# Performance work log

Hardware: AMD Instinct MI355X
Metric: run time of the kernel (lower is better)

The kernel has to match this reference:

```python
import jax, jax.numpy as jnp
import numpy as np

B, N, D, H, K, P, E = 4, 2048, 512, 8, 9, 8, 4
HID = 2048  # mlp_ratio * dim


def _ln(x, g, b, eps):
    m = x.mean(-1, keepdims=True)
    v = ((x - m) ** 2).mean(-1, keepdims=True)
    return (x - m) / jnp.sqrt(v + eps) * g + b


def _l2(x):
    # F.normalize(dim=-1)
    return x / jnp.maximum(jnp.linalg.norm(x, axis=-1, keepdims=True), 1e-12)


def _rope(t, pos):
    # t: [B,H,L,hd], rotate-half rotary embedding
    half = t.shape[-1] // 2
    inv = 1.0 / (10000.0 ** (jnp.arange(half, dtype=jnp.float32) / half))
    ang = pos[:, None].astype(jnp.float32) * inv  # [L, half]
    c, s = jnp.cos(ang), jnp.sin(ang)
    t1, t2 = t[..., :half], t[..., half:]
    return jnp.concatenate([t1 * c - t2 * s, t1 * s + t2 * c], axis=-1)


def setup_inputs() -> dict:
    key = jax.random.key(0)
    ks = jax.random.split(key, 12)
    w = lambda k, shape: jax.random.normal(k, shape, jnp.float32) * 0.02
    z = lambda *shape: jnp.zeros(shape, jnp.float32)
    o = lambda *shape: jnp.ones(shape, jnp.float32)
    return {
        'x': jax.random.normal(ks[0], (B, N, D), jnp.float32),
        'temperature': jnp.full((H, 1, 1), float(np.log(np.expm1(1.0 / 0.24))), jnp.float32),
        'q_w': w(ks[1], (D, D)), 'q_b': z(D),
        'kv_w': w(ks[2], (D, 2 * D)), 'kv_b': z(2 * D),
        'attn_proj_w': w(ks[3], (D, D)), 'attn_proj_b': z(D),
        'norm1_g': o(D), 'norm1_b': z(D),
        'norm2_g': o(D), 'norm2_b': z(D),
        'sr_w': w(ks[4], (D, D)), 'sr_b': z(D),  # Conv1d k=1 == pointwise linear
        'normp_g': o(D), 'normp_b': z(D),
        'router_w': w(ks[5], (D, E)), 'router_b': z(E),
        'ew1': w(ks[6], (E, D, HID)), 'eb1': z(E, HID),
        'ew2': w(ks[7], (E, HID, D)), 'eb2': z(E, D),
        'sw1': w(ks[8], (D, HID)), 'sb1': z(HID),
        'sw2': w(ks[9], (HID, D)), 'sb2': z(D),
    }


def _forward(x, temperature, q_w, q_b, kv_w, kv_b, attn_proj_w, attn_proj_b,
             norm1_g, norm1_b, norm2_g, norm2_b, sr_w, sr_b, normp_g, normp_b,
             router_w, router_b, ew1, eb1, ew2, eb2, sw1, sb1, sw2, sb2):
    Bn, Nn, Dd = x.shape
    hd = Dd // H
    scale_len = jnp.float32(np.log(K - 1 + P))  # log(local_len + pool_len)

    xn = _ln(x, norm1_g, norm1_b, 1e-6)
    q = (xn @ q_w + q_b).reshape(Bn, Nn, H, hd).transpose(0, 2, 1, 3)
    qs = _l2(q) * jax.nn.softplus(temperature) * scale_len  # [B,H,N,hd]
    kv = xn @ kv_w + kv_b
    kL = kv[..., :Dd].reshape(Bn, Nn, H, hd).transpose(0, 2, 1, 3)
    vL = kv[..., Dd:].reshape(Bn, Nn, H, hd).transpose(0, 2, 1, 3)
    pos = jnp.arange(Nn)
    qs = _rope(qs, pos)
    kL = _l2(_rope(kL, pos))

    # sliding-window local attention (qk with zero rpb; OOB positions -> -inf)
    offs = jnp.arange(K) - K // 2
    idx = jnp.arange(Nn)[:, None] + offs          # [N,K]
    valid = (idx >= 0) & (idx < Nn)
    idxc = jnp.clip(idx, 0, Nn - 1)
    kwin = kL[:, :, idxc, :]                       # [B,H,N,K,hd]
    attn_local = jnp.einsum('bhnd,bhnkd->bhnk', qs, kwin)
    attn_local = jnp.where(valid[None, None], attn_local, -jnp.inf)

    # pooled global branch: conv1x1 -> GELU -> adaptive avg pool -> LN
    xp = jax.nn.gelu(xn @ sr_w + sr_b, approximate=False)
    xp = xp.reshape(Bn, P, Nn // P, Dd).mean(2)    # AdaptiveAvgPool1d(P)
    xp = _ln(xp, normp_g, normp_b, 1e-5)
    kvp = xp @ kv_w + kv_b
    kP = kvp[..., :Dd].reshape(Bn, P, H, hd).transpose(0, 2, 1, 3)
    vP = kvp[..., Dd:].reshape(Bn, P, H, hd).transpose(0, 2, 1, 3)
    kP = _rope(kP, jnp.arange(P))
    attn_pool = jnp.einsum('bhnd,bhpd->bhnp', qs, kP)

    attn = jax.nn.softmax(jnp.concatenate([attn_local, attn_pool], -1), axis=-1)
    aL, aP = attn[..., :K], attn[..., K:]
    vwin = vL[:, :, idxc, :]
    xl = jnp.einsum('bhnk,bhnkd->bhnd', aL, vwin)
    xg = jnp.einsum('bhnp,bhpd->bhnd', aP, vP)
    attn_out = (xl + xg).transpose(0, 2, 1, 3).reshape(Bn, Nn, Dd)
    x = x + (attn_out @ attn_proj_w + attn_proj_b)

    # MoE with shared expert (dense soft gating + switch-style aux loss)
    xn2 = _ln(x, norm2_g, norm2_b, 1e-6)
    gates = jax.nn.softmax(xn2 @ router_w + router_b, axis=-1)  # [B,N,E]
    h = jax.nn.gelu(jnp.einsum('bnd,edh->bneh', xn2, ew1) + eb1, approximate=False)
    eo = jnp.einsum('bneh,ehd->bned', h, ew2) + eb2
    shared = jax.nn.gelu(xn2 @ sw1 + sb1, approximate=False) @ sw2 + sb2
    moe = jnp.einsum('bne,bned->bnd', gates, eo) + shared
    x = x + moe
    fi = jnp.mean(jax.nn.one_hot(jnp.argmax(gates, -1), E, dtype=jnp.float32), axis=(0, 1))
    Pi = jnp.mean(gates, axis=(0, 1))
    aux = jnp.float32(0.01) * E * jnp.sum(fi * Pi)
    return x, aux


def reference(x, temperature, q_w, q_b, kv_w, kv_b, attn_proj_w, attn_proj_b,
              norm1_g, norm1_b, norm2_g, norm2_b, sr_w, sr_b, normp_g, normp_b,
              router_w, router_b, ew1, eb1, ew2, eb2, sw1, sb1, sw2, sb2):
    return _forward(x, temperature, q_w, q_b, kv_w, kv_b, attn_proj_w, attn_proj_b,
                    norm1_g, norm1_b, norm2_g, norm2_b, sr_w, sr_b, normp_g, normp_b,
                    router_w, router_b, ew1, eb1, ew2, eb2, sw1, sb1, sw2, sb2)
```

## Files before the change

### kernel.cpp

```cpp
#include <hip/hip_runtime.h>
#include <hip/hip_bf16.h>
#include <math.h>

#define B_ 4
#define N_ 2048
#define D_ 512
#define H_ 8
#define HD_ 64
#define KW_ 9
#define P_ 8
#define E_ 4
#define HID_ 2048
#define TOK_ (B_*N_)

typedef __bf16 bf16x8 __attribute__((ext_vector_type(8)));
typedef float  f32x4  __attribute__((ext_vector_type(4)));

static __device__ __forceinline__ float wave_sum(float v){
#pragma unroll
  for(int off=32; off>0; off>>=1) v += __shfl_xor(v, off);
  return v;
}

static __device__ __forceinline__ float gelu_exact(float v){
  return 0.5f * v * (1.f + erff(v * 0.70710678118654752440f));
}

static __device__ __forceinline__ void split2(float v, unsigned short& h, unsigned short& l){
  __bf16 bh = (__bf16)v;
  float r = v - (float)bh;
  __bf16 bl = (__bf16)r;
  h = __builtin_bit_cast(unsigned short, bh);
  l = __builtin_bit_cast(unsigned short, bl);
}
static __device__ __forceinline__ float bf2f(unsigned short u){
  return (float)__builtin_bit_cast(__bf16, u);
}
static __device__ __forceinline__ unsigned short f2bf(float v){
  return __builtin_bit_cast(unsigned short, (__bf16)v);
}

static __device__ __forceinline__ void gload16(const unsigned short* g, unsigned short* l){
  __builtin_amdgcn_global_load_lds(
      (const __attribute__((address_space(1))) unsigned int*)g,
      (__attribute__((address_space(3))) unsigned int*)l, 16, 0, 0);
}

__global__ __launch_bounds__(256) void wconv_kernel(const float* __restrict__ W,
    unsigned short* __restrict__ Th, unsigned short* __restrict__ Tl, int K, int N)
{
  size_t ms = (size_t)K*N;
  const float* Wb = W + blockIdx.z*ms;
  unsigned short* Thb = Th + blockIdx.z*ms;
  unsigned short* Tlb = Tl + blockIdx.z*ms;
  __shared__ float tile[64][65];
  int n0 = blockIdx.x*64, k0 = blockIdx.y*64;
  int t = threadIdx.x;
  int c4 = (t&15)*4, r = t>>4;
#pragma unroll
  for(int pass=0; pass<4; ++pass){
    int k = r + pass*16;
    float4 v = *(const float4*)(Wb + (size_t)(k0+k)*N + n0 + c4);
    tile[k][c4]=v.x; tile[k][c4+1]=v.y; tile[k][c4+2]=v.z; tile[k][c4+3]=v.w;
  }
  __syncthreads();
#pragma unroll
  for(int pass=0; pass<4; ++pass){
    int n = r + pass*16;
    unsigned short h0,h1,h2,h3,l0,l1,l2,l3;
    split2(tile[c4+0][n], h0, l0);
    split2(tile[c4+1][n], h1, l1);
    split2(tile[c4+2][n], h2, l2);
    split2(tile[c4+3][n], h3, l3);
    *(ushort4*)(Thb + (size_t)(n0+n)*K + k0 + c4) = make_ushort4(h0,h1,h2,h3);
    *(ushort4*)(Tlb + (size_t)(n0+n)*K + k0 + c4) = make_ushort4(l0,l1,l2,l3);
  }
}

#define GEPI_PLAIN     0
#define GEPI_GELU_F32  1
#define GEPI_RESID     2

template<int EPI>
__global__ __launch_bounds__(256,2) void gemm_mfma(
    const unsigned short* __restrict__ Ah, const unsigned short* __restrict__ Al,
    const unsigned short* __restrict__ Bh, const unsigned short* __restrict__ Bl,
    const float* __restrict__ bias,
    float* __restrict__ out,
    int M, int K, int N,
    const float* __restrict__ resid)
{
  __shared__ unsigned short lds[4][128][64];
  int tid = threadIdx.x;
  int lane = tid & 63, w = tid >> 6;
  int wm = w >> 1, wn = w & 1;
  int nbx = gridDim.x;
  int nwg = nbx * gridDim.y;
  int orig = blockIdx.y*nbx + blockIdx.x;
  int cpx = nwg >> 3;
  int swz = (orig & 7)*cpx + (orig >> 3);
  int bx = swz % nbx, by = swz / nbx;
  int row0 = by*128, col0 = bx*128;
  int r15 = lane & 15, g = lane >> 4;
  const unsigned short* Pb;
  if      (w==0) Pb = Ah + (size_t)row0*K;
  else if (w==1) Pb = Al + (size_t)row0*K;
  else if (w==2) Pb = Bh + (size_t)col0*K;
  else           Pb = Bl + (size_t)col0*K;
  const unsigned short* Pl = Pb + (size_t)(lane>>3)*K + (lane&7)*8;

  f32x4 acc[4][4];
#pragma unroll
  for(int i=0;i<4;++i)
#pragma unroll
    for(int j=0;j<4;++j) acc[i][j] = (f32x4){0.f,0.f,0.f,0.f};

  for(int k0=0; k0<K; k0+=64){
    __syncthreads();
#pragma unroll
    for(int c=0;c<16;++c){
      gload16(Pl + (size_t)(c*8)*K + k0, &lds[w][c*8][0]);
    }
    __syncthreads();
#pragma unroll
    for(int ks=0; ks<2; ++ks){
      bf16x8 afh[4], afl[4], bfh[4], bfl[4];
#pragma unroll
      for(int mf=0; mf<4; ++mf){
        int row = wm*64 + mf*16 + r15;
        afh[mf] = *(const bf16x8*)&lds[0][row][(ks*4+g)*8];
        afl[mf] = *(const bf16x8*)&lds[1][row][(ks*4+g)*8];
      }
#pragma unroll
      for(int nf=0; nf<4; ++nf){
        int row = wn*64 + nf*16 + r15;
        bfh[nf] = *(const bf16x8*)&lds[2][row][(ks*4+g)*8];
        bfl[nf] = *(const bf16x8*)&lds[3][row][(ks*4+g)*8];
      }
#pragma unroll
      for(int mf=0; mf<4; ++mf)
#pragma unroll
        for(int nf=0; nf<4; ++nf){
          acc[mf][nf] = __builtin_amdgcn_mfma_f32_16x16x32_bf16(afh[mf], bfh[nf], acc[mf][nf], 0,0,0);
          acc[mf][nf] = __builtin_amdgcn_mfma_f32_16x16x32_bf16(afh[mf], bfl[nf], acc[mf][nf], 0,0,0);
          acc[mf][nf] = __builtin_amdgcn_mfma_f32_16x16x32_bf16(afl[mf], bfh[nf], acc[mf][nf], 0,0,0);
        }
    }
  }
#pragma unroll
  for(int mf=0; mf<4; ++mf){
#pragma unroll
    for(int nf=0; nf<4; ++nf){
      int col = col0 + wn*64 + nf*16 + r15;
      float bv = bias[col];
#pragma unroll
      for(int v=0; v<4; ++v){
        int row = row0 + wm*64 + mf*16 + g*4 + v;
        size_t o = (size_t)row*N + col;
        float val = acc[mf][nf][v] + bv;
        if      (EPI == GEPI_GELU_F32){ out[o] = gelu_exact(val); }
        else if (EPI == GEPI_RESID){ out[o] = val + resid[o]; }
        else { out[o] = val; }
      }
    }
  }
}

#define G2_GELU 0
#define G2_ACC  1

template<int EPI>
__global__ __launch_bounds__(256,4) void gemm_bf16(
    const unsigned short* __restrict__ Ah,
    const unsigned short* __restrict__ Bh,
    const float* __restrict__ bias,
    float* __restrict__ out, unsigned short* __restrict__ outh,
    int M, int K, int N,
    const float* __restrict__ gate, int gstride)
{
  __shared__ unsigned short lds[2][128][64];
  int tid = threadIdx.x;
  int lane = tid & 63, w = tid >> 6;
  int wm = w >> 1, wn = w & 1;
  int nbx = gridDim.x;
  int nwg = nbx * gridDim.y;
  int orig = blockIdx.y*nbx + blockIdx.x;
  int cpx = nwg >> 3;
  int swz = (orig & 7)*cpx + (orig >> 3);
  int bx = swz % nbx, by = swz / nbx;
  int row0 = by*128, col0 = bx*128;
  int r15 = lane & 15, g = lane >> 4;
  int plane = w >> 1, half = w & 1;
  const unsigned short* Pb = (plane==0) ? (Ah + (size_t)(row0+half*64)*K)
                                        : (Bh + (size_t)(col0+half*64)*K);
  const unsigned short* Pl = Pb + (size_t)(lane>>3)*K + (lane&7)*8;

  f32x4 acc[4][4];
#pragma unroll
  for(int i=0;i<4;++i)
#pragma unroll
    for(int j=0;j<4;++j) acc[i][j] = (f32x4){0.f,0.f,0.f,0.f};

  for(int k0=0; k0<K; k0+=64){
    __syncthreads();
#pragma unroll
    for(int c=0;c<8;++c){
      gload16(Pl + (size_t)(c*8)*K + k0, &lds[plane][half*64 + c*8][0]);
    }
    __syncthreads();
#pragma unroll
    for(int ks=0; ks<2; ++ks){
      bf16x8 af[4], bf[4];
#pragma unroll
      for(int mf=0; mf<4; ++mf)
        af[mf] = *(const bf16x8*)&lds[0][wm*64 + mf*16 + r15][(ks*4+g)*8];
#pragma unroll
      for(int nf=0; nf<4; ++nf)
        bf[nf] = *(const bf16x8*)&lds[1][wn*64 + nf*16 + r15][(ks*4+g)*8];
#pragma unroll
      for(int mf=0; mf<4; ++mf)
#pragma unroll
        for(int nf=0; nf<4; ++nf)
          acc[mf][nf] = __builtin_amdgcn_mfma_f32_16x16x32_bf16(af[mf], bf[nf], acc[mf][nf], 0,0,0);
    }
  }
#pragma unroll
  for(int mf=0; mf<4; ++mf){
#pragma unroll
    for(int nf=0; nf<4; ++nf){
      int col = col0 + wn*64 + nf*16 + r15;
      float bv = bias[col];
#pragma unroll
      for(int v=0; v<4; ++v){
        int row = row0 + wm*64 + mf*16 + g*4 + v;
        size_t o = (size_t)row*N + col;
        float val = acc[mf][nf][v] + bv;
        if (EPI == G2_GELU){ outh[o] = f2bf(gelu_exact(val)); }
        else {
          float gv = gate ? gate[(size_t)row*gstride] : 1.f;
          out[o] += gv * val;
        }
      }
    }
  }
}

#define EPI_PLAIN 0
template<int EPI>
__global__ __launch_bounds__(256) void gemm_f32(
    const float* __restrict__ A, const float* __restrict__ W,
    const float* __restrict__ bias, float* __restrict__ out,
    int M, int Kd, int Nw,
    const float* __restrict__ resid,
    const float* __restrict__ gate, int gstride)
{
  __shared__ __align__(16) float As[16][128];
  __shared__ __align__(16) float Bs[16][128];
  int tid = threadIdx.x;
  int tx = tid & 15, ty = tid >> 4;
  int row0 = blockIdx.y * 128, col0 = blockIdx.x * 128;
  float acc[8][8];
#pragma unroll
  for(int i=0;i<8;++i)
#pragma unroll
    for(int j=0;j<8;++j) acc[i][j]=0.f;

  for(int k0=0; k0<Kd; k0+=16){
#pragma unroll
    for(int i=0;i<2;++i){
      int f4 = tid*2+i;
      int r  = f4 >> 2;
      int kc = (f4 & 3) << 2;
      int gr = row0 + r;
      float4 v = make_float4(0.f,0.f,0.f,0.f);
      if (gr < M) v = *(const float4*)(A + (size_t)gr*Kd + k0 + kc);
      As[kc+0][r]=v.x; As[kc+1][r]=v.y; As[kc+2][r]=v.z; As[kc+3][r]=v.w;
    }
#pragma unroll
    for(int i=0;i<2;++i){
      int f4 = tid*2+i;
      int kr = f4 >> 5;
      int c  = (f4 & 31) << 2;
      *(float4*)&Bs[kr][c] = *(const float4*)(W + (size_t)(k0+kr)*Nw + col0 + c);
    }
    __syncthreads();
#pragma unroll
    for(int kk=0;kk<16;++kk){
      float a[8], b[8];
      float4 a0 = *(const float4*)&As[kk][ty*8];
      float4 a1 = *(const float4*)&As[kk][ty*8+4];
      a[0]=a0.x;a[1]=a0.y;a[2]=a0.z;a[3]=a0.w;
      a[4]=a1.x;a[5]=a1.y;a[6]=a1.z;a[7]=a1.w;
      float4 b0 = *(const float4*)&Bs[kk][tx*8];
      float4 b1 = *(const float4*)&Bs[kk][tx*8+4];
      b[0]=b0.x;b[1]=b0.y;b[2]=b0.z;b[3]=b0.w;
      b[4]=b1.x;b[5]=b1.y;b[6]=b1.z;b[7]=b1.w;
#pragma unroll
      for(int i=0;i<8;++i)
#pragma unroll
        for(int j=0;j<8;++j)
          acc[i][j] = fmaf(a[i], b[j], acc[i][j]);
    }
    __syncthreads();
  }
#pragma unroll
  for(int i=0;i<8;++i){
    int gr = row0 + ty*8 + i;
    if (gr >= M) continue;
    size_t rb = (size_t)gr * Nw;
#pragma unroll
    for(int j=0;j<8;++j){
      int gc = col0 + tx*8 + j;
      out[rb+gc] = acc[i][j] + bias[gc];
    }
  }
}

__global__ __launch_bounds__(256) void ln_split_kernel(const float* __restrict__ in,
    const float* __restrict__ g, const float* __restrict__ b,
    unsigned short* __restrict__ outh, unsigned short* __restrict__ outl, float eps)
{
  int r = blockIdx.x;
  int tid = threadIdx.x;
  const float* rp = in + (size_t)r * D_;
  float2 v = *(const float2*)(rp + tid*2);
  float s = v.x + v.y;
  float q = v.x*v.x + v.y*v.y;
  s = wave_sum(s); q = wave_sum(q);
  __shared__ float ss[4], qq[4];
  int wid = tid >> 6, lane = tid & 63;
  if(lane==0){ ss[wid]=s; qq[wid]=q; }
  __syncthreads();
  float S = ss[0]+ss[1]+ss[2]+ss[3];
  float Q = qq[0]+qq[1]+qq[2]+qq[3];
  float mean = S * (1.f/D_);
  float var = Q * (1.f/D_) - mean*mean;
  float rstd = rsqrtf(var + eps);
  int d = tid*2;
  float o0 = (v.x-mean)*rstd*g[d]   + b[d];
  float o1 = (v.y-mean)*rstd*g[d+1] + b[d+1];
  unsigned short h0,l0,h1,l1;
  split2(o0,h0,l0); split2(o1,h1,l1);
  *(ushort2*)(outh + (size_t)r*D_ + d) = make_ushort2(h0,h1);
  *(ushort2*)(outl + (size_t)r*D_ + d) = make_ushort2(l0,l1);
}

__global__ __launch_bounds__(256) void qs_post_kernel(float* __restrict__ q,
                                                      const float* __restrict__ temp)
{
  int tid = threadIdx.x;
  int gid = blockIdx.x*4 + (tid>>6);
  int dd  = tid & 63;
  int h = gid % H_;
  int n = (gid / H_) % N_;
  int b = gid / (H_*N_);
  size_t idx = ((size_t)(b*N_+n))*D_ + h*HD_ + dd;
  float v = q[idx];
  float ss = wave_sum(v*v);
  v = v / fmaxf(sqrtf(ss), 1e-12f);
  float t = temp[h];
  float sp = log1pf(expf(t));
  v *= sp * 2.77258872223978124f;
  float partner = __shfl_xor(v, 32);
  int i = dd & 31;
  float inv = 1.f / powf(10000.f, (float)i * (1.f/32.f));
  float ang = (float)n * inv;
  float s, c; sincosf(ang, &s, &c);
  q[idx] = (dd < 32) ? fmaf(v, c, -partner*s) : fmaf(partner, s, v*c);
}

__global__ __launch_bounds__(256) void k_post_kernel(const float* __restrict__ kvb,
                                                     float* __restrict__ kln)
{
  int tid = threadIdx.x;
  int gid = blockIdx.x*4 + (tid>>6);
  int dd  = tid & 63;
  int h = gid % H_;
  int n = (gid / H_) % N_;
  int b = gid / (H_*N_);
  float v = kvb[((size_t)(b*N_+n))*(2*D_) + h*HD_ + dd];
  float partner = __shfl_xor(v, 32);
  int i = dd & 31;
  float inv = 1.f / powf(10000.f, (float)i * (1.f/32.f));
  float ang = (float)n * inv;
  float s, c; sincosf(ang, &s, &c);
  float r = (dd < 32) ? fmaf(v, c, -partner*s) : fmaf(partner, s, v*c);
  float ss = wave_sum(r*r);
  r = r / fmaxf(sqrtf(ss), 1e-12f);
  kln[((size_t)(b*N_+n))*D_ + h*HD_ + dd] = r;
}

__global__ __launch_bounds__(256) void pool_ln_kernel(const float* __restrict__ src,
    const float* __restrict__ g, const float* __restrict__ b, float* __restrict__ xp)
{
  int bp = blockIdx.x;
  int bb = bp / P_, p = bp % P_;
  int tid = threadIdx.x;
  const float* base = src + ((size_t)(bb*N_ + p*(N_/P_)))*D_;
  float a0=0.f, a1=0.f;
  for(int i=0;i<N_/P_;++i){
    a0 += base[(size_t)i*D_ + tid];
    a1 += base[(size_t)i*D_ + tid + 256];
  }
  a0 *= (1.f/(N_/P_)); a1 *= (1.f/(N_/P_));
  float s = a0+a1, q = a0*a0+a1*a1;
  s = wave_sum(s); q = wave_sum(q);
  __shared__ float ss[4], qq[4];
  int wid = tid>>6, lane = tid&63;
  if(lane==0){ ss[wid]=s; qq[wid]=q; }
  __syncthreads();
  float S = ss[0]+ss[1]+ss[2]+ss[3];
  float Q = qq[0]+qq[1]+qq[2]+qq[3];
  float mean = S*(1.f/D_);
  float var  = Q*(1.f/D_) - mean*mean;
  float rstd = rsqrtf(var + 1e-5f);
  xp[(size_t)bp*D_ + tid]       = (a0-mean)*rstd*g[tid]     + b[tid];
  xp[(size_t)bp*D_ + tid + 256] = (a1-mean)*rstd*g[tid+256] + b[tid+256];
}

__global__ __launch_bounds__(512) void kp_rope_kernel(const float* __restrict__ kvp,
                                                      float* __restrict__ kpb)
{
  int bp = blockIdx.x;
  int d  = threadIdx.x;
  int dd = d & 63;
  int p  = bp % P_;
  float v = kvp[(size_t)bp*(2*D_) + d];
  float partner = __shfl_xor(v, 32);
  int i = dd & 31;
  float inv = 1.f / powf(10000.f, (float)i * (1.f/32.f));
  float ang = (float)p * inv;
  float s, c; sincosf(ang, &s, &c);
  kpb[(size_t)bp*D_ + d] = (dd < 32) ? fmaf(v, c, -partner*s) : fmaf(partner, s, v*c);
}

static __device__ __forceinline__ float dot4(float4 a, float4 b){
  return fmaf(a.x,b.x, fmaf(a.y,b.y, fmaf(a.z,b.z, a.w*b.w)));
}

__global__ __launch_bounds__(256) void attn_kernel(
    const float* __restrict__ qs, const float* __restrict__ kln,
    const float* __restrict__ kvb, const float* __restrict__ kpb,
    const float* __restrict__ kvp,
    unsigned short* __restrict__ outh, unsigned short* __restrict__ outl)
{
  int tid = threadIdx.x;
  int gid = blockIdx.x*32 + (tid>>3);
  int l   = tid & 7;
  int d0  = l*8;
  int h = gid % H_;
  int n = (gid / H_) % N_;
  int b = gid / (H_*N_);
  size_t tok = (size_t)(b*N_+n);
  const float* qp = qs + tok*D_ + h*HD_ + d0;
  float4 qa = *(const float4*)qp;
  float4 qb = *(const float4*)(qp+4);
  float lg[KW_+P_];
#pragma unroll
  for(int j=0;j<KW_;++j){
    int np  = n - KW_/2 + j;
    int npc = min(max(np,0), N_-1);
    const float* kp = kln + ((size_t)(b*N_+npc))*D_ + h*HD_ + d0;
    float4 ka = *(const float4*)kp;
    float4 kb = *(const float4*)(kp+4);
    float d = dot4(qa,ka) + dot4(qb,kb);
#pragma unroll
    for(int off=1; off<8; off<<=1) d += __shfl_xor(d, off);
    lg[j] = (np>=0 && np<N_) ? d : -3.0e38f;
  }
#pragma unroll
  for(int p=0;p<P_;++p){
    const float* kp = kpb + ((size_t)(b*P_+p))*D_ + h*HD_ + d0;
    float4 ka = *(const float4*)kp;
    float4 kb = *(const float4*)(kp+4);
    float d = dot4(qa,ka) + dot4(qb,kb);
#pragma unroll
    for(int off=1; off<8; off<<=1) d += __shfl_xor(d, off);
    lg[KW_+p] = d;
  }
  float m = lg[0];
#pragma unroll
  for(int j=1;j<KW_+P_;++j) m = fmaxf(m, lg[j]);
  float a[KW_+P_]; float sum = 0.f;
#pragma unroll
  for(int j=0;j<KW_+P_;++j){ a[j] = expf(lg[j]-m); sum += a[j]; }
  float inv = 1.f / sum;
  float4 oa = make_float4(0.f,0.f,0.f,0.f);
  float4 ob = make_float4(0.f,0.f,0.f,0.f);
#pragma unroll
  for(int j=0;j<KW_;++j){
    int npc = min(max(n - KW_/2 + j, 0), N_-1);
    const float* vp = kvb + ((size_t)(b*N_+npc))*(2*D_) + D_ + h*HD_ + d0;
    float4 va = *(const float4*)vp;
    float4 vb = *(const float4*)(vp+4);
    oa.x=fmaf(a[j],va.x,oa.x); oa.y=fmaf(a[j],va.y,oa.y); oa.z=fmaf(a[j],va.z,oa.z); oa.w=fmaf(a[j],va.w,oa.w);
    ob.x=fmaf(a[j],vb.x,ob.x); ob.y=fmaf(a[j],vb.y,ob.y); ob.z=fmaf(a[j],vb.z,ob.z); ob.w=fmaf(a[j],vb.w,ob.w);
  }
#pragma unroll
  for(int p=0;p<P_;++p){
    float w = a[KW_+p];
    const float* vp = kvp + ((size_t)(b*P_+p))*(2*D_) + D_ + h*HD_ + d0;
    float4 va = *(const float4*)vp;
    float4 vb = *(const float4*)(vp+4);
    oa.x=fmaf(w,va.x,oa.x); oa.y=fmaf(w,va.y,oa.y); oa.z=fmaf(w,va.z,oa.z); oa.w=fmaf(w,va.w,oa.w);
    ob.x=fmaf(w,vb.x,ob.x); ob.y=fmaf(w,vb.y,ob.y); ob.z=fmaf(w,vb.z,ob.z); ob.w=fmaf(w,vb.w,ob.w);
  }
  unsigned short h0,h1,h2,h3,l0,l1,l2,l3;
  size_t ob_ = tok*D_ + h*HD_ + d0;
  split2(oa.x*inv,h0,l0); split2(oa.y*inv,h1,l1); split2(oa.z*inv,h2,l2); split2(oa.w*inv,h3,l3);
  *(ushort4*)(outh + ob_)   = make_ushort4(h0,h1,h2,h3);
  *(ushort4*)(outl + ob_)   = make_ushort4(l0,l1,l2,l3);
  split2(ob.x*inv,h0,l0); split2(ob.y*inv,h1,l1); split2(ob.z*inv,h2,l2); split2(ob.w*inv,h3,l3);
  *(ushort4*)(outh + ob_+4) = make_ushort4(h0,h1,h2,h3);
  *(ushort4*)(outl + ob_+4) = make_ushort4(l0,l1,l2,l3);
}

__global__ void zero_stats_kernel(float* stats){
  if(threadIdx.x < 16) stats[threadIdx.x] = 0.f;
}

__global__ __launch_bounds__(256) void router_kernel(
    const unsigned short* __restrict__ xh, const unsigned short* __restrict__ xl,
    const float* __restrict__ rw, const float* __restrict__ rb,
    float* __restrict__ gates, float* __restrict__ stats)
{
  int tid = threadIdx.x;
  int wid = tid>>6, lane = tid&63;
  int t = blockIdx.x*4 + wid;
  float a0=0.f,a1=0.f,a2=0.f,a3=0.f;
  for(int k=lane;k<D_;k+=64){
    float xv = bf2f(xh[(size_t)t*D_+k]) + bf2f(xl[(size_t)t*D_+k]);
    float4 w = *(const float4*)(rw + (size_t)k*E_);
    a0 = fmaf(xv,w.x,a0); a1 = fmaf(xv,w.y,a1);
    a2 = fmaf(xv,w.z,a2); a3 = fmaf(xv,w.w,a3);
  }
  a0=wave_sum(a0); a1=wave_sum(a1); a2=wave_sum(a2); a3=wave_sum(a3);
  __shared__ float sg[4][E_], sc[4][E_];
  if(lane==0){
    float lg[E_] = {a0+rb[0], a1+rb[1], a2+rb[2], a3+rb[3]};
    float m = fmaxf(fmaxf(lg[0],lg[1]), fmaxf(lg[2],lg[3]));
    float e[E_]; float sum=0.f;
#pragma unroll
    for(int k=0;k<E_;++k){ e[k]=expf(lg[k]-m); sum+=e[k]; }
    float inv = 1.f/sum;
    int am = 0; float bv = lg[0];
#pragma unroll
    for(int k=1;k<E_;++k) if(lg[k] > bv){ bv = lg[k]; am = k; }
#pragma unroll
    for(int k=0;k<E_;++k){
      float gk = e[k]*inv;
      gates[(size_t)t*E_ + k] = gk;
      sg[wid][k] = gk;
      sc[wid][k] = (k==am) ? 1.f : 0.f;
    }
  }
  __syncthreads();
  if(tid < E_){
    atomicAdd(stats + tid,      sc[0][tid]+sc[1][tid]+sc[2][tid]+sc[3][tid]);
    atomicAdd(stats + E_ + tid, sg[0][tid]+sg[1][tid]+sg[2][tid]+sg[3][tid]);
  }
}

__global__ void aux_kernel(const float* __restrict__ stats, float* __restrict__ outp){
  float acc = 0.f;
  const float inv = 1.f / (float)TOK_;
#pragma unroll
  for(int e=0;e<E_;++e) acc += (stats[e]*inv) * (stats[E_+e]*inv);
  *outp = 0.01f * (float)E_ * acc;
}

extern "C" void kernel_launch(void* const* d_in, const int* in_sizes, int n_in,
                              void* d_out, int out_size, void* d_ws, size_t ws_size,
                              hipStream_t stream)
{
  const float* x      = (const float*)d_in[0];
  const float* temp   = (const float*)d_in[1];
  const float* q_w    = (const float*)d_in[2];
  const float* q_b    = (const float*)d_in[3];
  const float* kv_w   = (const float*)d_in[4];
  const float* kv_b   = (const float*)d_in[5];
  const float* proj_w = (const float*)d_in[6];
  const float* proj_b = (const float*)d_in[7];
  const float* n1g    = (const float*)d_in[8];
  const float* n1b    = (const float*)d_in[9];
  const float* n2g    = (const float*)d_in[10];
  const float* n2b    = (const float*)d_in[11];
  const float* sr_w   = (const float*)d_in[12];
  const float* sr_b   = (const float*)d_in[13];
  const float* npg    = (const float*)d_in[14];
  const float* npb    = (const float*)d_in[15];
  const float* rw     = (const float*)d_in[16];
  const float* rb     = (const float*)d_in[17];
  const float* ew1    = (const float*)d_in[18];
  const float* eb1    = (const float*)d_in[19];
  const float* ew2    = (const float*)d_in[20];
  const float* eb2    = (const float*)d_in[21];
  const float* sw1    = (const float*)d_in[22];
  const float* sb1    = (const float*)d_in[23];
  const float* sw2    = (const float*)d_in[24];
  const float* sb2    = (const float*)d_in[25];

  float* out = (float*)d_out;
  const size_t S = (size_t)TOK_ * D_;
  char* base = (char*)d_ws;
  size_t off = 0;
  auto aus = [&](size_t n)->unsigned short*{ unsigned short* p=(unsigned short*)(base+off); off += n*2; return p; };
  auto af  = [&](size_t n)->float*{ float* p=(float*)(base+off); off += n*4; return p; };

  unsigned short *qwh = aus(512*512),  *qwl = aus(512*512);
  unsigned short *kvwh= aus(512*1024), *kvwl= aus(512*1024);
  unsigned short *srwh= aus(512*512),  *srwl= aus(512*512);
  unsigned short *pjwh= aus(512*512),  *pjwl= aus(512*512);
  unsigned short *s1h = aus(512*2048), *s1l = aus(512*2048);
  unsigned short *s2h = aus(2048*512), *s2l = aus(2048*512);
  unsigned short *e1h = aus((size_t)E_*512*2048), *e1l = aus((size_t)E_*512*2048);
  unsigned short *e2h = aus((size_t)E_*2048*512), *e2l = aus((size_t)E_*2048*512);
  unsigned short *xnh = aus(S), *xnl = aus(S);
  float* qsb = af(S);
  float* kvb = af(2*S);
  float* kln = af(S);
  unsigned short* hidh = (unsigned short*)qsb;
  float* srg = af(S);
  unsigned short* atth = (unsigned short*)srg;
  unsigned short* attl = atth + S;
  float* xp    = af((size_t)B_*P_*D_);
  float* kvp   = af((size_t)B_*P_*2*D_);
  float* kpb   = af((size_t)B_*P_*D_);
  float* gates = af((size_t)TOK_*E_);
  float* stats = af(16);

  wconv_kernel<<<dim3(8,8,1),  256, 0, stream>>>(q_w,    qwh, qwl, 512, 512);
  wconv_kernel<<<dim3(16,8,1), 256, 0, stream>>>(kv_w,   kvwh,kvwl,512, 1024);
  wconv_kernel<<<dim3(8,8,1),  256, 0, stream>>>(sr_w,   srwh,srwl,512, 512);
  wconv_kernel<<<dim3(8,8,1),  256, 0, stream>>>(proj_w, pjwh,pjwl,512, 512);
  wconv_kernel<<<dim3(32,8,1), 256, 0, stream>>>(sw1,    s1h, s1l, 512, 2048);
  wconv_kernel<<<dim3(8,32,1), 256, 0, stream>>>(sw2,    s2h, s2l, 2048,512);
  wconv_kernel<<<dim3(32,8,E_),256, 0, stream>>>(ew1,    e1h, e1l, 512, 2048);
  wconv_kernel<<<dim3(8,32,E_),256, 0, stream>>>(ew2,    e2h, e2l, 2048,512);

  ln_split_kernel<<<dim3(TOK_), 256, 0, stream>>>(x, n1g, n1b, xnh, xnl, 1e-6f);
  gemm_mfma<GEPI_PLAIN><<<dim3(4,64), 256, 0, stream>>>(xnh,xnl,qwh,qwl,q_b, qsb, TOK_,512,512, nullptr);
  gemm_mfma<GEPI_PLAIN><<<dim3(8,64), 256, 0, stream>>>(xnh,xnl,kvwh,kvwl,kv_b, kvb, TOK_,512,1024, nullptr);
  gemm_mfma<GEPI_GELU_F32><<<dim3(4,64), 256, 0, stream>>>(xnh,xnl,srwh,srwl,sr_b, srg, TOK_,512,512, nullptr);
  pool_ln_kernel<<<dim3(B_*P_), 256, 0, stream>>>(srg, npg, npb, xp);
  gemm_f32<EPI_PLAIN><<<dim3(8,1), 256, 0, stream>>>(xp, kv_w, kv_b, kvp, B_*P_, 512, 1024, nullptr, nullptr, 0);
  kp_rope_kernel<<<dim3(B_*P_), 512, 0, stream>>>(kvp, kpb);
  qs_post_kernel<<<dim3(B_*N_*H_/4), 256, 0, stream>>>(qsb, temp);
  k_post_kernel<<<dim3(B_*N_*H_/4), 256, 0, stream>>>(kvb, kln);
  attn_kernel<<<dim3(B_*H_*N_/32), 256, 0, stream>>>(qsb, kln, kvb, kpb, kvp, atth, attl);
  gemm_mfma<GEPI_RESID><<<dim3(4,64), 256, 0, stream>>>(atth,attl,pjwh,pjwl,proj_b, out, TOK_,512,512, x);
  ln_split_kernel<<<dim3(TOK_), 256, 0, stream>>>(out, n2g, n2b, xnh, xnl, 1e-6f);
  zero_stats_kernel<<<dim3(1), 64, 0, stream>>>(stats);
  router_kernel<<<dim3(TOK_/4), 256, 0, stream>>>(xnh, xnl, rw, rb, gates, stats);
  gemm_bf16<G2_GELU><<<dim3(16,64), 256, 0, stream>>>(xnh, s1h, sb1, nullptr, hidh, TOK_,512,HID_, nullptr,0);
  gemm_bf16<G2_ACC ><<<dim3(4,64),  256, 0, stream>>>(hidh, s2h, sb2, out, nullptr, TOK_,HID_,512, nullptr,0);
  for(int e=0;e<E_;++e){
    gemm_bf16<G2_GELU><<<dim3(16,64), 256, 0, stream>>>(xnh, e1h+(size_t)e*512*2048, eb1+(size_t)e*HID_, nullptr, hidh, TOK_,512,HID_, nullptr,0);
    gemm_bf16<G2_ACC ><<<dim3(4,64),  256, 0, stream>>>(hidh, e2h+(size_t)e*2048*512, eb2+(size_t)e*D_, out, nullptr, TOK_,HID_,512, gates+e,E_);
  }
  aux_kernel<<<dim3(1), 1, 0, stream>>>(stats, out + S);
}
```

Baseline: 945.5 us.

## Halve split-bf16 GEMM K-tile for occupancy, replace tiny fp32 GEMM, cheaper RoPE freqs

The split-precision MFMA GEMM now stages a 32-wide K slice instead of 64, halving its LDS footprint, and its launch bounds ask for 4 workgroups per CU instead of 2, trading more barriers per K step for more resident waves. The 32-row pooled KV projection, which used a 128x128 fp32 tile that wasted most of its rows, is replaced by a simple per-output-column dot-product kernel with more blocks. The RoPE inverse frequency is computed with exp2f and a precomputed constant instead of powf and a division. The GEMM change risks extra synchronization overhead and register pressure under the higher occupancy target.

```diff
diff --git a/kernel.cpp b/kernel.cpp
--- a/kernel.cpp
+++ b/kernel.cpp
@@ -16,6 +16,8 @@
 typedef __bf16 bf16x8 __attribute__((ext_vector_type(8)));
 typedef float  f32x4  __attribute__((ext_vector_type(4)));
 
+#define LOG2_10000_OVER_32 0.41524101186092034f
+
 static __device__ __forceinline__ float wave_sum(float v){
 #pragma unroll
   for(int off=32; off>0; off>>=1) v += __shfl_xor(v, off);
@@ -82,7 +84,7 @@
 #define GEPI_RESID     2
 
 template<int EPI>
-__global__ __launch_bounds__(256,2) void gemm_mfma(
+__global__ __launch_bounds__(256,4) void gemm_mfma(
     const unsigned short* __restrict__ Ah, const unsigned short* __restrict__ Al,
     const unsigned short* __restrict__ Bh, const unsigned short* __restrict__ Bl,
     const float* __restrict__ bias,
@@ -90,7 +92,7 @@
     int M, int K, int N,
     const float* __restrict__ resid)
 {
-  __shared__ unsigned short lds[4][128][64];
+  __shared__ unsigned short lds[4][128][32];
   int tid = threadIdx.x;
   int lane = tid & 63, w = tid >> 6;
   int wm = w >> 1, wn = w & 1;
@@ -107,7 +109,7 @@
   else if (w==1) Pb = Al + (size_t)row0*K;
   else if (w==2) Pb = Bh + (size_t)col0*K;
   else           Pb = Bl + (size_t)col0*K;
-  const unsigned short* Pl = Pb + (size_t)(lane>>3)*K + (lane&7)*8;
+  const unsigned short* Pl = Pb + (size_t)(lane>>2)*K + (lane&3)*8;
 
   f32x4 acc[4][4];
 #pragma unroll
@@ -115,37 +117,34 @@
 #pragma unroll
     for(int j=0;j<4;++j) acc[i][j] = (f32x4){0.f,0.f,0.f,0.f};
 
-  for(int k0=0; k0<K; k0+=64){
+  for(int k0=0; k0<K; k0+=32){
     __syncthreads();
 #pragma unroll
-    for(int c=0;c<16;++c){
-      gload16(Pl + (size_t)(c*8)*K + k0, &lds[w][c*8][0]);
+    for(int c=0;c<8;++c){
+      gload16(Pl + (size_t)(c*16)*K + k0, &lds[w][c*16][0]);
     }
     __syncthreads();
-#pragma unroll
-    for(int ks=0; ks<2; ++ks){
-      bf16x8 afh[4], afl[4], bfh[4], bfl[4];
-#pragma unroll
-      for(int mf=0; mf<4; ++mf){
-        int row = wm*64 + mf*16 + r15;
-        afh[mf] = *(const bf16x8*)&lds[0][row][(ks*4+g)*8];
-        afl[mf] = *(const bf16x8*)&lds[1][row][(ks*4+g)*8];
+    bf16x8 afh[4], afl[4], bfh[4], bfl[4];
+#pragma unroll
+    for(int mf=0; mf<4; ++mf){
+      int row = wm*64 + mf*16 + r15;
+      afh[mf] = *(const bf16x8*)&lds[0][row][g*8];
+      afl[mf] = *(const bf16x8*)&lds[1][row][g*8];
+    }
+#pragma unroll
+    for(int nf=0; nf<4; ++nf){
+      int row = wn*64 + nf*16 + r15;
+      bfh[nf] = *(const bf16x8*)&lds[2][row][g*8];
+      bfl[nf] = *(const bf16x8*)&lds[3][row][g*8];
+    }
+#pragma unroll
+    for(int mf=0; mf<4; ++mf)
+#pragma unroll
+      for(int nf=0; nf<4; ++nf){
+        acc[mf][nf] = __builtin_amdgcn_mfma_f32_16x16x32_bf16(afh[mf], bfh[nf], acc[mf][nf], 0,0,0);
+        acc[mf][nf] = __builtin_amdgcn_mfma_f32_16x16x32_bf16(afh[mf], bfl[nf], acc[mf][nf], 0,0,0);
+        acc[mf][nf] = __builtin_amdgcn_mfma_f32_16x16x32_bf16(afl[mf], bfh[nf], acc[mf][nf], 0,0,0);
       }
-#pragma unroll
-      for(int nf=0; nf<4; ++nf){
-        int row = wn*64 + nf*16 + r15;
-        bfh[nf] = *(const bf16x8*)&lds[2][row][(ks*4+g)*8];
-        bfl[nf] = *(const bf16x8*)&lds[3][row][(ks*4+g)*8];
-      }
-#pragma unroll
-      for(int mf=0; mf<4; ++mf)
-#pragma unroll
-        for(int nf=0; nf<4; ++nf){
-          acc[mf][nf] = __builtin_amdgcn_mfma_f32_16x16x32_bf16(afh[mf], bfh[nf], acc[mf][nf], 0,0,0);
-          acc[mf][nf] = __builtin_amdgcn_mfma_f32_16x16x32_bf16(afh[mf], bfl[nf], acc[mf][nf], 0,0,0);
-          acc[mf][nf] = __builtin_amdgcn_mfma_f32_16x16x32_bf16(afl[mf], bfh[nf], acc[mf][nf], 0,0,0);
-        }
-    }
   }
 #pragma unroll
   for(int mf=0; mf<4; ++mf){
@@ -245,75 +244,22 @@
   }
 }
 
-#define EPI_PLAIN 0
-template<int EPI>
-__global__ __launch_bounds__(256) void gemm_f32(
-    const float* __restrict__ A, const float* __restrict__ W,
-    const float* __restrict__ bias, float* __restrict__ out,
-    int M, int Kd, int Nw,
-    const float* __restrict__ resid,
-    const float* __restrict__ gate, int gstride)
-{
-  __shared__ __align__(16) float As[16][128];
-  __shared__ __align__(16) float Bs[16][128];
-  int tid = threadIdx.x;
-  int tx = tid & 15, ty = tid >> 4;
-  int row0 = blockIdx.y * 128, col0 = blockIdx.x * 128;
-  float acc[8][8];
-#pragma unroll
-  for(int i=0;i<8;++i)
-#pragma unroll
-    for(int j=0;j<8;++j) acc[i][j]=0.f;
-
-  for(int k0=0; k0<Kd; k0+=16){
-#pragma unroll
-    for(int i=0;i<2;++i){
-      int f4 = tid*2+i;
-      int r  = f4 >> 2;
-      int kc = (f4 & 3) << 2;
-      int gr = row0 + r;
-      float4 v = make_float4(0.f,0.f,0.f,0.f);
-      if (gr < M) v = *(const float4*)(A + (size_t)gr*Kd + k0 + kc);
-      As[kc+0][r]=v.x; As[kc+1][r]=v.y; As[kc+2][r]=v.z; As[kc+3][r]=v.w;
-    }
-#pragma unroll
-    for(int i=0;i<2;++i){
-      int f4 = tid*2+i;
-      int kr = f4 >> 5;
-      int c  = (f4 & 31) << 2;
-      *(float4*)&Bs[kr][c] = *(const float4*)(W + (size_t)(k0+kr)*Nw + col0 + c);
-    }
-    __syncthreads();
-#pragma unroll
-    for(int kk=0;kk<16;++kk){
-      float a[8], b[8];
-      float4 a0 = *(const float4*)&As[kk][ty*8];
-      float4 a1 = *(const float4*)&As[kk][ty*8+4];
-      a[0]=a0.x;a[1]=a0.y;a[2]=a0.z;a[3]=a0.w;
-      a[4]=a1.x;a[5]=a1.y;a[6]=a1.z;a[7]=a1.w;
-      float4 b0 = *(const float4*)&Bs[kk][tx*8];
-      float4 b1 = *(const float4*)&Bs[kk][tx*8+4];
-      b[0]=b0.x;b[1]=b0.y;b[2]=b0.z;b[3]=b0.w;
-      b[4]=b1.x;b[5]=b1.y;b[6]=b1.z;b[7]=b1.w;
-#pragma unroll
-      for(int i=0;i<8;++i)
-#pragma unroll
-        for(int j=0;j<8;++j)
-          acc[i][j] = fmaf(a[i], b[j], acc[i][j]);
-    }
-    __syncthreads();
-  }
-#pragma unroll
-  for(int i=0;i<8;++i){
-    int gr = row0 + ty*8 + i;
-    if (gr >= M) continue;
-    size_t rb = (size_t)gr * Nw;
-#pragma unroll
-    for(int j=0;j<8;++j){
-      int gc = col0 + tx*8 + j;
-      out[rb+gc] = acc[i][j] + bias[gc];
-    }
-  }
+__global__ __launch_bounds__(256) void kvp_small_kernel(
+    const float* __restrict__ xp, const float* __restrict__ W,
+    const float* __restrict__ bias, float* __restrict__ out)
+{
+  __shared__ float xr[512];
+  int row = blockIdx.y;
+  int col = blockIdx.x*256 + threadIdx.x;
+  float2 v = *(const float2*)(xp + (size_t)row*512 + threadIdx.x*2);
+  xr[threadIdx.x*2]   = v.x;
+  xr[threadIdx.x*2+1] = v.y;
+  __syncthreads();
+  float acc = 0.f;
+#pragma unroll 8
+  for(int k=0;k<512;++k)
+    acc = fmaf(xr[k], W[(size_t)k*1024 + col], acc);
+  out[(size_t)row*1024 + col] = acc + bias[col];
 }
 
 __global__ __launch_bounds__(256) void ln_split_kernel(const float* __restrict__ in,
@@ -363,7 +309,7 @@
   v *= sp * 2.77258872223978124f;
   float partner = __shfl_xor(v, 32);
   int i = dd & 31;
-  float inv = 1.f / powf(10000.f, (float)i * (1.f/32.f));
+  float inv = exp2f(-(float)i * LOG2_10000_OVER_32);
   float ang = (float)n * inv;
   float s, c; sincosf(ang, &s, &c);
   q[idx] = (dd < 32) ? fmaf(v, c, -partner*s) : fmaf(partner, s, v*c);
@@ -381,7 +327,7 @@
   float v = kvb[((size_t)(b*N_+n))*(2*D_) + h*HD_ + dd];
   float partner = __shfl_xor(v, 32);
   int i = dd & 31;
-  float inv = 1.f / powf(10000.f, (float)i * (1.f/32.f));
+  float inv = exp2f(-(float)i * LOG2_10000_OVER_32);
   float ang = (float)n * inv;
   float s, c; sincosf(ang, &s, &c);
   float r = (dd < 32) ? fmaf(v, c, -partner*s) : fmaf(partner, s, v*c);
@@ -428,7 +374,7 @@
   float v = kvp[(size_t)bp*(2*D_) + d];
   float partner = __shfl_xor(v, 32);
   int i = dd & 31;
-  float inv = 1.f / powf(10000.f, (float)i * (1.f/32.f));
+  float inv = exp2f(-(float)i * LOG2_10000_OVER_32);
   float ang = (float)p * inv;
   float s, c; sincosf(ang, &s, &c);
   kpb[(size_t)bp*D_ + d] = (dd < 32) ? fmaf(v, c, -partner*s) : fmaf(partner, s, v*c);
@@ -643,7 +589,7 @@
   gemm_mfma<GEPI_PLAIN><<<dim3(8,64), 256, 0, stream>>>(xnh,xnl,kvwh,kvwl,kv_b, kvb, TOK_,512,1024, nullptr);
   gemm_mfma<GEPI_GELU_F32><<<dim3(4,64), 256, 0, stream>>>(xnh,xnl,srwh,srwl,sr_b, srg, TOK_,512,512, nullptr);
   pool_ln_kernel<<<dim3(B_*P_), 256, 0, stream>>>(srg, npg, npb, xp);
-  gemm_f32<EPI_PLAIN><<<dim3(8,1), 256, 0, stream>>>(xp, kv_w, kv_b, kvp, B_*P_, 512, 1024, nullptr, nullptr, 0);
+  kvp_small_kernel<<<dim3(4,32), 256, 0, stream>>>(xp, kv_w, kv_b, kvp);
   kp_rope_kernel<<<dim3(B_*P_), 512, 0, stream>>>(kvp, kpb);
   qs_post_kernel<<<dim3(B_*N_*H_/4), 256, 0, stream>>>(qsb, temp);
   k_post_kernel<<<dim3(B_*N_*H_/4), 256, 0, stream>>>(kvb, kln);
```

Result: no change. 937.9 us (-0.8%).
